# Performance work log

Hardware: AMD Instinct MI355X
Metric: run time of the kernel (lower is better)

## Reference

```python
import jax, jax.numpy as jnp
import numpy as np

Y, Z, H, R = 32, 64, 256, 256  # y_dim, z_dim, h_dim, rnn_dim
T, B = 200, 2048


def setup_inputs() -> dict:
    key = jax.random.key(0)
    ks = jax.random.split(key, 32)
    w = lambda k, shape: jax.random.normal(k, shape, jnp.float32) * 0.05
    z32 = lambda n: jnp.zeros((n,), jnp.float32)
    return {
        "states": jax.random.normal(ks[0], (T, B, Y), jnp.float32),
        "eps": jax.random.normal(ks[1], (T - 1, B, Z), jnp.float32),
        # encoder q(z|x,y,h): Linear(2Y+R,H) ReLU Linear(H,H) ReLU
        "enc_w1": w(ks[2], (H, 2 * Y + R)), "enc_b1": z32(H),
        "enc_w2": w(ks[3], (H, H)), "enc_b2": z32(H),
        "enc_mw": w(ks[4], (Z, H)), "enc_mb": z32(Z),
        "enc_sw": w(ks[5], (Z, H)), "enc_sb": z32(Z),
        # prior p(z|y,h): Linear(Y+R,H) ReLU Linear(H,H) ReLU
        "pri_w1": w(ks[6], (H, Y + R)), "pri_b1": z32(H),
        "pri_w2": w(ks[7], (H, H)), "pri_b2": z32(H),
        "pri_mw": w(ks[8], (Z, H)), "pri_mb": z32(Z),
        "pri_sw": w(ks[9], (Z, H)), "pri_sb": z32(Z),
        # decoder p(x|y,z,h): Linear(Y+Z+R,H) ReLU Linear(H,H) ReLU
        "dec_w1": w(ks[10], (H, Y + Z + R)), "dec_b1": z32(H),
        "dec_w2": w(ks[11], (H, H)), "dec_b2": z32(H),
        "dec_mw": w(ks[12], (Y, H)), "dec_mb": z32(Y),
        "dec_sw": w(ks[13], (Y, H)), "dec_sb": z32(Y),
        # GRU(Y+Z -> R), 1 layer; torch gate order [r, z, n]
        "gru_wih": w(ks[14], (3 * R, Y + Z)), "gru_whh": w(ks[15], (3 * R, R)),
        "gru_bih": z32(3 * R), "gru_bhh": z32(3 * R),
    }


def reference(states, eps, enc_w1, enc_b1, enc_w2, enc_b2, enc_mw, enc_mb,
              enc_sw, enc_sb, pri_w1, pri_b1, pri_w2, pri_b2, pri_mw, pri_mb,
              pri_sw, pri_sb, dec_w1, dec_b1, dec_w2, dec_b2, dec_mw, dec_mb,
              dec_sw, dec_sb, gru_wih, gru_whh, gru_bih, gru_bhh):
    batch = states.shape[1]
    rnn_dim = gru_whh.shape[1]
    relu, sp = jax.nn.relu, jax.nn.softplus
    LOG2PI = jnp.float32(np.log(2.0 * np.pi))

    def mlp2(x, w1, b1, w2, b2):
        return relu(relu(x @ w1.T + b1) @ w2.T + b2)

    def step(h, inp):
        y, x, e = inp  # y=states[t], x=states[t+1], e: reparam noise
        enc_h = mlp2(jnp.concatenate([x, y, h], 1), enc_w1, enc_b1, enc_w2, enc_b2)
        em = enc_h @ enc_mw.T + enc_mb
        es = sp(enc_h @ enc_sw.T + enc_sb)
        pri_h = mlp2(jnp.concatenate([y, h], 1), pri_w1, pri_b1, pri_w2, pri_b2)
        pm = pri_h @ pri_mw.T + pri_mb
        ps = sp(pri_h @ pri_sw.T + pri_sb)
        z = em + es * e  # sample_gauss
        dec_h = mlp2(jnp.concatenate([y, z, h], 1), dec_w1, dec_b1, dec_w2, dec_b2)
        dm = dec_h @ dec_mw.T + dec_mb
        ds = sp(dec_h @ dec_sw.T + dec_sb)
        # GRU cell (torch gate order r,z,n)
        gi = jnp.concatenate([x, z], 1) @ gru_wih.T + gru_bih
        gh = h @ gru_whh.T + gru_bhh
        ir, iz, inn = jnp.split(gi, 3, axis=1)
        hr, hz, hn = jnp.split(gh, 3, axis=1)
        r = jax.nn.sigmoid(ir + hr)
        u = jax.nn.sigmoid(iz + hz)
        n = jnp.tanh(inn + r * hn)
        h_new = (1.0 - u) * n + u * h
        kl = 0.5 * jnp.sum(2.0 * jnp.log(ps / es) + (es ** 2 + (em - pm) ** 2) / ps ** 2 - 1.0)
        nll = jnp.sum(jnp.log(ds) + (x - dm) ** 2 / (2.0 * ds ** 2) + 0.5 * LOG2PI)
        return h_new, (kl, nll)

    h0 = jnp.zeros((batch, rnn_dim), states.dtype)
    _, (kls, nlls) = jax.lax.scan(step, h0, (states[:-1], states[1:], eps))
    # out = [kl_loss, recon_loss]
    return jnp.stack([jnp.sum(kls), jnp.sum(nlls)])
```

## Files before the change

kernel.cpp:

```cpp
#include <hip/hip_runtime.h>

typedef unsigned short u16;
typedef unsigned int u32;
typedef __bf16 bf16x8 __attribute__((ext_vector_type(8)));
typedef float f32x4 __attribute__((ext_vector_type(4)));

#define YD 32
#define ZD 64
#define HD 256
#define RD 256
#define TSTEPS 199
#define BB 2048
#define MROWS 32
#define NBLK 64
#define NTHR 512
#define CATS 392
#define HBS  264

enum : int {
  OFF_ENC_W1 = 0,
  OFF_ENC_W2 = 81920,
  OFF_ENC_H  = 147456,
  OFF_PRI_W1 = 180224,
  OFF_PRI_W2 = 253952,
  OFF_PRI_H  = 319488,
  OFF_DEC_W1 = 352256,
  OFF_DEC_W2 = 442368,
  OFF_DEC_H  = 507904,
  OFF_GWIH   = 524288,
  OFF_GWHH   = 598016,
};

__device__ __forceinline__ u16 f2bf(float f) {
  u32 u = __float_as_uint(f);
  u += 0x7fffu + ((u >> 16) & 1u);
  return (u16)(u >> 16);
}
__device__ __forceinline__ float softplus_f(float x) {
  float l = __logf(1.f + __expf(-fabsf(x)));
  return x > 0.f ? x + l : l;
}
__device__ __forceinline__ float sigmoid_f(float x) {
  return __builtin_amdgcn_rcpf(1.f + __expf(-x));
}
__device__ __forceinline__ float tanh_f(float x) {
  float e = __expf(-2.f * fabsf(x));
  float t = (1.f - e) * __builtin_amdgcn_rcpf(1.f + e);
  return x >= 0.f ? t : -t;
}

template<int NT, int RT, int KS, int AS>
__device__ __forceinline__ void gemm_seg(f32x4 (&acc)[NT][RT],
    const u16* __restrict__ W, const int Kw, const int wrow0, const int wk0,
    const u16* A, const int acol0, const int rt0, const int lane)
{
  const int n = lane & 15, quad = lane >> 4;
  #pragma unroll
  for (int ks = 0; ks < KS; ++ks) {
    bf16x8 a[RT];
    #pragma unroll
    for (int rt = 0; rt < RT; ++rt)
      a[rt] = *reinterpret_cast<const bf16x8*>(A + ((rt0 + rt) * 16 + n) * AS + acol0 + ks * 32 + quad * 8);
    #pragma unroll
    for (int nt = 0; nt < NT; ++nt) {
      bf16x8 b = *reinterpret_cast<const bf16x8*>(W + (size_t)(wrow0 + nt * 16 + n) * Kw + wk0 + ks * 32 + quad * 8);
      #pragma unroll
      for (int rt = 0; rt < RT; ++rt)
        acc[nt][rt] = __builtin_amdgcn_mfma_f32_16x16x32_bf16(a[rt], b, acc[nt][rt], 0, 0, 0);
    }
  }
}

template<int NT, int RT, int DS>
__device__ __forceinline__ void store_relu(const f32x4 (&acc)[NT][RT], u16* dst,
    const int col0, const int rt0, const float* __restrict__ bias, const int lane)
{
  const int n = lane & 15, quad = lane >> 4;
  #pragma unroll
  for (int nt = 0; nt < NT; ++nt) {
    const float b = bias[col0 + nt * 16 + n];
    #pragma unroll
    for (int rt = 0; rt < RT; ++rt)
      #pragma unroll
      for (int i = 0; i < 4; ++i) {
        float v = fmaxf(acc[nt][rt][i] + b, 0.f);
        dst[((rt0 + rt) * 16 + quad * 4 + i) * DS + col0 + nt * 16 + n] = f2bf(v);
      }
  }
}

struct PrepArgs { const float* src[14]; int off[14]; int cnt[14]; };

__global__ void prep_weights(PrepArgs a, u16* __restrict__ dst) {
  const int j = blockIdx.y;
  const float* __restrict__ s = a.src[j];
  u16* d = dst + a.off[j];
  const int nel = a.cnt[j];
  for (int i = blockIdx.x * blockDim.x + threadIdx.x; i < nel; i += gridDim.x * blockDim.x)
    d[i] = f2bf(s[i]);
}

__global__ void zero_out_k(float* out) { if (threadIdx.x < 2) out[threadIdx.x] = 0.f; }

__global__ __launch_bounds__(NTHR, 1)
void vrnn_kernel(const float* __restrict__ states, const float* __restrict__ eps,
                 const float* __restrict__ enc_b1, const float* __restrict__ enc_b2,
                 const float* __restrict__ enc_mb, const float* __restrict__ enc_sb,
                 const float* __restrict__ pri_b1, const float* __restrict__ pri_b2,
                 const float* __restrict__ pri_mb, const float* __restrict__ pri_sb,
                 const float* __restrict__ dec_b1, const float* __restrict__ dec_b2,
                 const float* __restrict__ dec_mb, const float* __restrict__ dec_sb,
                 const float* __restrict__ gbih, const float* __restrict__ gbhh,
                 const u16* __restrict__ ws, float* __restrict__ out)
{
  __shared__ u16 cat[MROWS * CATS];
  __shared__ u16 hb1[MROWS * HBS];
  __shared__ u16 hb2[MROWS * HBS];

  const int tid = threadIdx.x;
  const int w = tid >> 6, lane = tid & 63;
  const int n = lane & 15, quad = lane >> 4;
  const int r0 = blockIdx.x * MROWS;
  const int n0 = w * 32;
  const int ctH = w & 3, rtH = w >> 2;

  for (int i = tid; i < MROWS * (HD / 2); i += NTHR) {
    int row = i >> 7, c = (i & 127) * 2;
    *reinterpret_cast<u32*>(&cat[row * CATS + 128 + c]) = 0u;
  }

  float hreg[2][2][4];
  #pragma unroll
  for (int a = 0; a < 2; ++a)
    #pragma unroll
    for (int b = 0; b < 2; ++b)
      #pragma unroll
      for (int c = 0; c < 4; ++c) hreg[a][b][c] = 0.f;

  float kl_acc = 0.f, nll_acc = 0.f;
  float emv[4], esv[4];

  for (int t = 0; t < TSTEPS; ++t) {
    {
      const int tt = tid & 255, row = tt >> 3, c4 = (tt & 7) * 4;
      const size_t tsel = (tid < 256) ? (size_t)(t + 1) : (size_t)t;
      const float4 v = *reinterpret_cast<const float4*>(states + (tsel * BB + r0 + row) * YD + c4);
      u16* d = cat + row * CATS + ((tid < 256) ? 0 : 32) + c4;
      d[0] = f2bf(v.x); d[1] = f2bf(v.y); d[2] = f2bf(v.z); d[3] = f2bf(v.w);
    }
    __syncthreads();

    {
      f32x4 acc[2][2] = {};
      gemm_seg<2, 2, 2, CATS>(acc, ws + OFF_ENC_W1, 320, n0, 0, cat, 0, 0, lane);
      gemm_seg<2, 2, 8, CATS>(acc, ws + OFF_ENC_W1, 320, n0, 64, cat, 128, 0, lane);
      store_relu<2, 2, HBS>(acc, hb1, n0, 0, enc_b1, lane);
    }
    __syncthreads();

    {
      f32x4 acc[2][2] = {};
      gemm_seg<2, 2, 8, HBS>(acc, ws + OFF_ENC_W2, 256, n0, 0, hb1, 0, 0, lane);
      store_relu<2, 2, HBS>(acc, hb2, n0, 0, enc_b2, lane);
    }
    __syncthreads();

    {
      f32x4 am[1][1] = {}, as[1][1] = {};
      gemm_seg<1, 1, 8, HBS>(am, ws + OFF_ENC_H, 256, ctH * 16, 0, hb2, 0, rtH, lane);
      gemm_seg<1, 1, 8, HBS>(as, ws + OFF_ENC_H, 256, 64 + ctH * 16, 0, hb2, 0, rtH, lane);
      const int j = ctH * 16 + n;
      #pragma unroll
      for (int i = 0; i < 4; ++i) {
        const int m = rtH * 16 + quad * 4 + i;
        float em = am[0][0][i] + enc_mb[j];
        float es = softplus_f(as[0][0][i] + enc_sb[j]);
        emv[i] = em; esv[i] = es;
        float e = eps[((size_t)t * BB + r0 + m) * ZD + j];
        cat[m * CATS + 64 + j] = f2bf(em + es * e);
      }
      f32x4 acc[2][2] = {};
      gemm_seg<2, 2, 1, CATS>(acc, ws + OFF_PRI_W1, 288, n0, 0, cat, 32, 0, lane);
      gemm_seg<2, 2, 8, CATS>(acc, ws + OFF_PRI_W1, 288, n0, 32, cat, 128, 0, lane);
      store_relu<2, 2, HBS>(acc, hb1, n0, 0, pri_b1, lane);
    }
    __syncthreads();

    {
      f32x4 acc[2][2] = {};
      gemm_seg<2, 2, 8, HBS>(acc, ws + OFF_PRI_W2, 256, n0, 0, hb1, 0, 0, lane);
      store_relu<2, 2, HBS>(acc, hb2, n0, 0, pri_b2, lane);
    }
    __syncthreads();

    {
      f32x4 am[1][1] = {}, as[1][1] = {};
      gemm_seg<1, 1, 8, HBS>(am, ws + OFF_PRI_H, 256, ctH * 16, 0, hb2, 0, rtH, lane);
      gemm_seg<1, 1, 8, HBS>(as, ws + OFF_PRI_H, 256, 64 + ctH * 16, 0, hb2, 0, rtH, lane);
      const int j = ctH * 16 + n;
      #pragma unroll
      for (int i = 0; i < 4; ++i) {
        float pm = am[0][0][i] + pri_mb[j];
        float ps = softplus_f(as[0][0][i] + pri_sb[j]);
        float es = esv[i], em = emv[i];
        float d = em - pm;
        kl_acc += 0.5f * (2.f * __logf(ps * __builtin_amdgcn_rcpf(es))
                          + (es * es + d * d) / (ps * ps) - 1.f);
      }
      f32x4 acc[2][2] = {};
      gemm_seg<2, 2, 3, CATS>(acc, ws + OFF_DEC_W1, 352, n0, 0, cat, 32, 0, lane);
      gemm_seg<2, 2, 8, CATS>(acc, ws + OFF_DEC_W1, 352, n0, 96, cat, 128, 0, lane);
      store_relu<2, 2, HBS>(acc, hb1, n0, 0, dec_b1, lane);
    }
    __syncthreads();

    {
      f32x4 acc[2][2] = {};
      gemm_seg<2, 2, 8, HBS>(acc, ws + OFF_DEC_W2, 256, n0, 0, hb1, 0, 0, lane);
      store_relu<2, 2, HBS>(acc, hb2, n0, 0, dec_b2, lane);
    }
    __syncthreads();

    {
      if (w < 4) {
        const int p = w & 1, rtb = w >> 1;
        f32x4 am[1][1] = {}, as[1][1] = {};
        gemm_seg<1, 1, 8, HBS>(am, ws + OFF_DEC_H, 256, p * 16, 0, hb2, 0, rtb, lane);
        gemm_seg<1, 1, 8, HBS>(as, ws + OFF_DEC_H, 256, 32 + p * 16, 0, hb2, 0, rtb, lane);
        const int j = p * 16 + n;
        #pragma unroll
        for (int i = 0; i < 4; ++i) {
          const int m = rtb * 16 + quad * 4 + i;
          float dm = am[0][0][i] + dec_mb[j];
          float ds = softplus_f(as[0][0][i] + dec_sb[j]);
          float xv = states[((size_t)(t + 1) * BB + r0 + m) * YD + j];
          float dd = xv - dm;
          nll_acc += __logf(ds) + dd * dd / (2.f * ds * ds) + 0.91893853320467274178f;
        }
      }
      f32x4 aR[2][2] = {}, aU[2][2] = {}, aN[2][2] = {}, aH[2][2] = {};
      gemm_seg<2, 2, 1, CATS>(aR, ws + OFF_GWIH, 96, n0, 0, cat, 0, 0, lane);
      gemm_seg<2, 2, 2, CATS>(aR, ws + OFF_GWIH, 96, n0, 32, cat, 64, 0, lane);
      gemm_seg<2, 2, 8, CATS>(aR, ws + OFF_GWHH, 256, n0, 0, cat, 128, 0, lane);
      gemm_seg<2, 2, 1, CATS>(aU, ws + OFF_GWIH, 96, RD + n0, 0, cat, 0, 0, lane);
      gemm_seg<2, 2, 2, CATS>(aU, ws + OFF_GWIH, 96, RD + n0, 32, cat, 64, 0, lane);
      gemm_seg<2, 2, 8, CATS>(aU, ws + OFF_GWHH, 256, RD + n0, 0, cat, 128, 0, lane);
      gemm_seg<2, 2, 1, CATS>(aN, ws + OFF_GWIH, 96, 2 * RD + n0, 0, cat, 0, 0, lane);
      gemm_seg<2, 2, 2, CATS>(aN, ws + OFF_GWIH, 96, 2 * RD + n0, 32, cat, 64, 0, lane);
      gemm_seg<2, 2, 8, CATS>(aH, ws + OFF_GWHH, 256, 2 * RD + n0, 0, cat, 128, 0, lane);
      #pragma unroll
      for (int nt = 0; nt < 2; ++nt) {
        const int j = n0 + nt * 16 + n;
        const float br = gbih[j] + gbhh[j];
        const float bu = gbih[RD + j] + gbhh[RD + j];
        const float bin = gbih[2 * RD + j];
        const float bhn = gbhh[2 * RD + j];
        #pragma unroll
        for (int rt = 0; rt < 2; ++rt)
          #pragma unroll
          for (int i = 0; i < 4; ++i) {
            float r = sigmoid_f(aR[nt][rt][i] + br);
            float u = sigmoid_f(aU[nt][rt][i] + bu);
            float nn = tanh_f(aN[nt][rt][i] + bin + r * (aH[nt][rt][i] + bhn));
            hreg[nt][rt][i] = (1.f - u) * nn + u * hreg[nt][rt][i];
          }
      }
    }
    __syncthreads();

    #pragma unroll
    for (int nt = 0; nt < 2; ++nt)
      #pragma unroll
      for (int rt = 0; rt < 2; ++rt)
        #pragma unroll
        for (int i = 0; i < 4; ++i)
          cat[(rt * 16 + quad * 4 + i) * CATS + 128 + n0 + nt * 16 + n] = f2bf(hreg[nt][rt][i]);
  }

  float kv = kl_acc, nv = nll_acc;
  #pragma unroll
  for (int off = 32; off > 0; off >>= 1) {
    kv += __shfl_down(kv, off, 64);
    nv += __shfl_down(nv, off, 64);
  }
  if (lane == 0) {
    atomicAdd(out + 0, kv);
    atomicAdd(out + 1, nv);
  }
}

extern "C" void kernel_launch(void* const* d_in, const int* in_sizes, int n_in,
                              void* d_out, int out_size, void* d_ws, size_t ws_size,
                              hipStream_t stream) {
  const float* states = (const float*)d_in[0];
  const float* eps    = (const float*)d_in[1];
  u16* ws   = (u16*)d_ws;
  float* out = (float*)d_out;

  PrepArgs pa;
  const int jsrc[14] = {2, 4, 6, 8, 10, 12, 14, 16, 18, 20, 22, 24, 26, 27};
  const int joff[14] = {OFF_ENC_W1, OFF_ENC_W2, OFF_ENC_H, OFF_ENC_H + 16384,
                        OFF_PRI_W1, OFF_PRI_W2, OFF_PRI_H, OFF_PRI_H + 16384,
                        OFF_DEC_W1, OFF_DEC_W2, OFF_DEC_H, OFF_DEC_H + 8192,
                        OFF_GWIH, OFF_GWHH};
  const int jcnt[14] = {81920, 65536, 16384, 16384,
                        73728, 65536, 16384, 16384,
                        90112, 65536, 8192, 8192,
                        73728, 196608};
  for (int j = 0; j < 14; ++j) {
    pa.src[j] = (const float*)d_in[jsrc[j]];
    pa.off[j] = joff[j];
    pa.cnt[j] = jcnt[j];
  }

  zero_out_k<<<dim3(1), dim3(64), 0, stream>>>(out);
  prep_weights<<<dim3(64, 14), dim3(256), 0, stream>>>(pa, ws);
  vrnn_kernel<<<dim3(NBLK), dim3(NTHR), 0, stream>>>(
      states, eps,
      (const float*)d_in[3],  (const float*)d_in[5],
      (const float*)d_in[7],  (const float*)d_in[9],
      (const float*)d_in[11], (const float*)d_in[13],
      (const float*)d_in[15], (const float*)d_in[17],
      (const float*)d_in[19], (const float*)d_in[21],
      (const float*)d_in[23], (const float*)d_in[25],
      (const float*)d_in[28], (const float*)d_in[29],
      ws, out);
}
```

Measured before the change: 11.13 ms.

## Double rows per block to reuse weights and prefetch per-step inputs

Each block now handles 64 batch rows instead of 32, so every weight fragment loaded from global memory feeds four row tiles of MFMAs instead of two. This halves the grid to 32 blocks. Biases are hoisted into registers, the next step's states and the current eps/x values are prefetched ahead of the GEMMs, and the GRU gate computation is reordered to reduce live accumulator registers. The cost is fewer blocks on a large GPU, larger LDS buffers and more register pressure, all on a latency-bound recurrent loop.

```diff
diff --git a/kernel.cpp b/kernel.cpp
--- a/kernel.cpp
+++ b/kernel.cpp
@@ -11,8 +11,8 @@
 #define RD 256
 #define TSTEPS 199
 #define BB 2048
-#define MROWS 32
-#define NBLK 64
+#define MROWS 64
+#define NBLK 32
 #define NTHR 512
 #define CATS 392
 #define HBS  264
@@ -73,12 +73,12 @@
 
 template<int NT, int RT, int DS>
 __device__ __forceinline__ void store_relu(const f32x4 (&acc)[NT][RT], u16* dst,
-    const int col0, const int rt0, const float* __restrict__ bias, const int lane)
+    const int col0, const int rt0, const float* bias_r, const int lane)
 {
   const int n = lane & 15, quad = lane >> 4;
   #pragma unroll
   for (int nt = 0; nt < NT; ++nt) {
-    const float b = bias[col0 + nt * 16 + n];
+    const float b = bias_r[nt];
     #pragma unroll
     for (int rt = 0; rt < RT; ++rt)
       #pragma unroll
@@ -102,7 +102,7 @@
 
 __global__ void zero_out_k(float* out) { if (threadIdx.x < 2) out[threadIdx.x] = 0.f; }
 
-__global__ __launch_bounds__(NTHR, 1)
+__global__ __launch_bounds__(NTHR, 2)
 void vrnn_kernel(const float* __restrict__ states, const float* __restrict__ eps,
                  const float* __restrict__ enc_b1, const float* __restrict__ enc_b2,
                  const float* __restrict__ enc_mb, const float* __restrict__ enc_sb,
@@ -122,156 +122,203 @@
   const int n = lane & 15, quad = lane >> 4;
   const int r0 = blockIdx.x * MROWS;
   const int n0 = w * 32;
-  const int ctH = w & 3, rtH = w >> 2;
+  const int ctH = w & 3, rtH0 = (w >> 2) * 2;
+  const int pD = w & 1, rtD = w >> 1;
+
+  float b1e[2], b2e[2], b1p[2], b2p[2], b1d[2], b2d[2];
+  float brg[2], bug[2], bing[2], bhng[2];
+  #pragma unroll
+  for (int nt = 0; nt < 2; ++nt) {
+    const int j = n0 + nt * 16 + n;
+    b1e[nt] = enc_b1[j]; b2e[nt] = enc_b2[j];
+    b1p[nt] = pri_b1[j]; b2p[nt] = pri_b2[j];
+    b1d[nt] = dec_b1[j]; b2d[nt] = dec_b2[j];
+    brg[nt] = gbih[j] + gbhh[j];
+    bug[nt] = gbih[RD + j] + gbhh[RD + j];
+    bing[nt] = gbih[2 * RD + j];
+    bhng[nt] = gbhh[2 * RD + j];
+  }
+  const int jH = ctH * 16 + n;
+  const float bem = enc_mb[jH], bes = enc_sb[jH];
+  const float bpm = pri_mb[jH], bps = pri_sb[jH];
+  const int jD = pD * 16 + n;
+  const float bdm = dec_mb[jD], bds = dec_sb[jD];
 
   for (int i = tid; i < MROWS * (HD / 2); i += NTHR) {
     int row = i >> 7, c = (i & 127) * 2;
     *reinterpret_cast<u32*>(&cat[row * CATS + 128 + c]) = 0u;
   }
 
-  float hreg[2][2][4];
+  float hreg[2][4][4];
   #pragma unroll
   for (int a = 0; a < 2; ++a)
     #pragma unroll
-    for (int b = 0; b < 2; ++b)
+    for (int b = 0; b < 4; ++b)
       #pragma unroll
       for (int c = 0; c < 4; ++c) hreg[a][b][c] = 0.f;
 
+  const int srow = tid >> 3, sc4 = (tid & 7) * 4;
+  float4 xf = *reinterpret_cast<const float4*>(states + ((size_t)1 * BB + r0 + srow) * YD + sc4);
+  float4 yf = *reinterpret_cast<const float4*>(states + ((size_t)0 * BB + r0 + srow) * YD + sc4);
+
   float kl_acc = 0.f, nll_acc = 0.f;
-  float emv[4], esv[4];
 
   for (int t = 0; t < TSTEPS; ++t) {
     {
-      const int tt = tid & 255, row = tt >> 3, c4 = (tt & 7) * 4;
-      const size_t tsel = (tid < 256) ? (size_t)(t + 1) : (size_t)t;
-      const float4 v = *reinterpret_cast<const float4*>(states + (tsel * BB + r0 + row) * YD + c4);
-      u16* d = cat + row * CATS + ((tid < 256) ? 0 : 32) + c4;
-      d[0] = f2bf(v.x); d[1] = f2bf(v.y); d[2] = f2bf(v.z); d[3] = f2bf(v.w);
-    }
-    __syncthreads();
-
-    {
-      f32x4 acc[2][2] = {};
-      gemm_seg<2, 2, 2, CATS>(acc, ws + OFF_ENC_W1, 320, n0, 0, cat, 0, 0, lane);
-      gemm_seg<2, 2, 8, CATS>(acc, ws + OFF_ENC_W1, 320, n0, 64, cat, 128, 0, lane);
-      store_relu<2, 2, HBS>(acc, hb1, n0, 0, enc_b1, lane);
-    }
-    __syncthreads();
-
-    {
-      f32x4 acc[2][2] = {};
-      gemm_seg<2, 2, 8, HBS>(acc, ws + OFF_ENC_W2, 256, n0, 0, hb1, 0, 0, lane);
-      store_relu<2, 2, HBS>(acc, hb2, n0, 0, enc_b2, lane);
+      u16* dx = cat + srow * CATS + sc4;
+      dx[0] = f2bf(xf.x); dx[1] = f2bf(xf.y); dx[2] = f2bf(xf.z); dx[3] = f2bf(xf.w);
+      u16* dy = cat + srow * CATS + 32 + sc4;
+      dy[0] = f2bf(yf.x); dy[1] = f2bf(yf.y); dy[2] = f2bf(yf.z); dy[3] = f2bf(yf.w);
+    }
+    __syncthreads();
+
+    float ev[2][4];
+    #pragma unroll
+    for (int rt = 0; rt < 2; ++rt)
+      #pragma unroll
+      for (int i = 0; i < 4; ++i)
+        ev[rt][i] = eps[((size_t)t * BB + r0 + (rtH0 + rt) * 16 + quad * 4 + i) * ZD + jH];
+    float xs[4];
+    #pragma unroll
+    for (int i = 0; i < 4; ++i)
+      xs[i] = states[((size_t)(t + 1) * BB + r0 + rtD * 16 + quad * 4 + i) * YD + jD];
+
+    {
+      f32x4 acc[2][4] = {};
+      gemm_seg<2, 4, 2, CATS>(acc, ws + OFF_ENC_W1, 320, n0, 0, cat, 0, 0, lane);
+      gemm_seg<2, 4, 8, CATS>(acc, ws + OFF_ENC_W1, 320, n0, 64, cat, 128, 0, lane);
+      store_relu<2, 4, HBS>(acc, hb1, n0, 0, b1e, lane);
+    }
+    __syncthreads();
+
+    {
+      f32x4 acc[2][4] = {};
+      gemm_seg<2, 4, 8, HBS>(acc, ws + OFF_ENC_W2, 256, n0, 0, hb1, 0, 0, lane);
+      store_relu<2, 4, HBS>(acc, hb2, n0, 0, b2e, lane);
+    }
+    __syncthreads();
+
+    float emv[2][4], esv[2][4];
+    {
+      f32x4 am[1][2] = {}, as[1][2] = {};
+      gemm_seg<1, 2, 8, HBS>(am, ws + OFF_ENC_H, 256, ctH * 16, 0, hb2, 0, rtH0, lane);
+      gemm_seg<1, 2, 8, HBS>(as, ws + OFF_ENC_H, 256, 64 + ctH * 16, 0, hb2, 0, rtH0, lane);
+      #pragma unroll
+      for (int rt = 0; rt < 2; ++rt)
+        #pragma unroll
+        for (int i = 0; i < 4; ++i) {
+          const int m = (rtH0 + rt) * 16 + quad * 4 + i;
+          float em = am[0][rt][i] + bem;
+          float es = softplus_f(as[0][rt][i] + bes);
+          emv[rt][i] = em; esv[rt][i] = es;
+          cat[m * CATS + 64 + jH] = f2bf(em + es * ev[rt][i]);
+        }
+      f32x4 acc[2][4] = {};
+      gemm_seg<2, 4, 1, CATS>(acc, ws + OFF_PRI_W1, 288, n0, 0, cat, 32, 0, lane);
+      gemm_seg<2, 4, 8, CATS>(acc, ws + OFF_PRI_W1, 288, n0, 32, cat, 128, 0, lane);
+      store_relu<2, 4, HBS>(acc, hb1, n0, 0, b1p, lane);
+    }
+    __syncthreads();
+
+    {
+      f32x4 acc[2][4] = {};
+      gemm_seg<2, 4, 8, HBS>(acc, ws + OFF_PRI_W2, 256, n0, 0, hb1, 0, 0, lane);
+      store_relu<2, 4, HBS>(acc, hb2, n0, 0, b2p, lane);
+    }
+    __syncthreads();
+
+    {
+      f32x4 am[1][2] = {}, as[1][2] = {};
+      gemm_seg<1, 2, 8, HBS>(am, ws + OFF_PRI_H, 256, ctH * 16, 0, hb2, 0, rtH0, lane);
+      gemm_seg<1, 2, 8, HBS>(as, ws + OFF_PRI_H, 256, 64 + ctH * 16, 0, hb2, 0, rtH0, lane);
+      #pragma unroll
+      for (int rt = 0; rt < 2; ++rt)
+        #pragma unroll
+        for (int i = 0; i < 4; ++i) {
+          float pm = am[0][rt][i] + bpm;
+          float ps = softplus_f(as[0][rt][i] + bps);
+          float es = esv[rt][i], em = emv[rt][i];
+          float d = em - pm;
+          kl_acc += 0.5f * (2.f * __logf(ps * __builtin_amdgcn_rcpf(es))
+                            + (es * es + d * d) / (ps * ps) - 1.f);
+        }
+      f32x4 acc[2][4] = {};
+      gemm_seg<2, 4, 3, CATS>(acc, ws + OFF_DEC_W1, 352, n0, 0, cat, 32, 0, lane);
+      gemm_seg<2, 4, 8, CATS>(acc, ws + OFF_DEC_W1, 352, n0, 96, cat, 128, 0, lane);
+      store_relu<2, 4, HBS>(acc, hb1, n0, 0, b1d, lane);
+    }
+    __syncthreads();
+
+    {
+      f32x4 acc[2][4] = {};
+      gemm_seg<2, 4, 8, HBS>(acc, ws + OFF_DEC_W2, 256, n0, 0, hb1, 0, 0, lane);
+      store_relu<2, 4, HBS>(acc, hb2, n0, 0, b2d, lane);
     }
     __syncthreads();
 
     {
       f32x4 am[1][1] = {}, as[1][1] = {};
-      gemm_seg<1, 1, 8, HBS>(am, ws + OFF_ENC_H, 256, ctH * 16, 0, hb2, 0, rtH, lane);
-      gemm_seg<1, 1, 8, HBS>(as, ws + OFF_ENC_H, 256, 64 + ctH * 16, 0, hb2, 0, rtH, lane);
-      const int j = ctH * 16 + n;
+      gemm_seg<1, 1, 8, HBS>(am, ws + OFF_DEC_H, 256, pD * 16, 0, hb2, 0, rtD, lane);
+      gemm_seg<1, 1, 8, HBS>(as, ws + OFF_DEC_H, 256, 32 + pD * 16, 0, hb2, 0, rtD, lane);
       #pragma unroll
       for (int i = 0; i < 4; ++i) {
-        const int m = rtH * 16 + quad * 4 + i;
-        float em = am[0][0][i] + enc_mb[j];
-        float es = softplus_f(as[0][0][i] + enc_sb[j]);
-        emv[i] = em; esv[i] = es;
-        float e = eps[((size_t)t * BB + r0 + m) * ZD + j];
-        cat[m * CATS + 64 + j] = f2bf(em + es * e);
-      }
-      f32x4 acc[2][2] = {};
-      gemm_seg<2, 2, 1, CATS>(acc, ws + OFF_PRI_W1, 288, n0, 0, cat, 32, 0, lane);
-      gemm_seg<2, 2, 8, CATS>(acc, ws + OFF_PRI_W1, 288, n0, 32, cat, 128, 0, lane);
-      store_relu<2, 2, HBS>(acc, hb1, n0, 0, pri_b1, lane);
-    }
-    __syncthreads();
-
-    {
-      f32x4 acc[2][2] = {};
-      gemm_seg<2, 2, 8, HBS>(acc, ws + OFF_PRI_W2, 256, n0, 0, hb1, 0, 0, lane);
-      store_relu<2, 2, HBS>(acc, hb2, n0, 0, pri_b2, lane);
-    }
-    __syncthreads();
-
-    {
-      f32x4 am[1][1] = {}, as[1][1] = {};
-      gemm_seg<1, 1, 8, HBS>(am, ws + OFF_PRI_H, 256, ctH * 16, 0, hb2, 0, rtH, lane);
-      gemm_seg<1, 1, 8, HBS>(as, ws + OFF_PRI_H, 256, 64 + ctH * 16, 0, hb2, 0, rtH, lane);
-      const int j = ctH * 16 + n;
-      #pragma unroll
-      for (int i = 0; i < 4; ++i) {
-        float pm = am[0][0][i] + pri_mb[j];
-        float ps = softplus_f(as[0][0][i] + pri_sb[j]);
-        float es = esv[i], em = emv[i];
-        float d = em - pm;
-        kl_acc += 0.5f * (2.f * __logf(ps * __builtin_amdgcn_rcpf(es))
-                          + (es * es + d * d) / (ps * ps) - 1.f);
-      }
-      f32x4 acc[2][2] = {};
-      gemm_seg<2, 2, 3, CATS>(acc, ws + OFF_DEC_W1, 352, n0, 0, cat, 32, 0, lane);
-      gemm_seg<2, 2, 8, CATS>(acc, ws + OFF_DEC_W1, 352, n0, 96, cat, 128, 0, lane);
-      store_relu<2, 2, HBS>(acc, hb1, n0, 0, dec_b1, lane);
-    }
-    __syncthreads();
-
-    {
-      f32x4 acc[2][2] = {};
-      gemm_seg<2, 2, 8, HBS>(acc, ws + OFF_DEC_W2, 256, n0, 0, hb1, 0, 0, lane);
-      store_relu<2, 2, HBS>(acc, hb2, n0, 0, dec_b2, lane);
-    }
-    __syncthreads();
-
-    {
-      if (w < 4) {
-        const int p = w & 1, rtb = w >> 1;
-        f32x4 am[1][1] = {}, as[1][1] = {};
-        gemm_seg<1, 1, 8, HBS>(am, ws + OFF_DEC_H, 256, p * 16, 0, hb2, 0, rtb, lane);
-        gemm_seg<1, 1, 8, HBS>(as, ws + OFF_DEC_H, 256, 32 + p * 16, 0, hb2, 0, rtb, lane);
-        const int j = p * 16 + n;
-        #pragma unroll
-        for (int i = 0; i < 4; ++i) {
-          const int m = rtb * 16 + quad * 4 + i;
-          float dm = am[0][0][i] + dec_mb[j];
-          float ds = softplus_f(as[0][0][i] + dec_sb[j]);
-          float xv = states[((size_t)(t + 1) * BB + r0 + m) * YD + j];
-          float dd = xv - dm;
-          nll_acc += __logf(ds) + dd * dd / (2.f * ds * ds) + 0.91893853320467274178f;
-        }
-      }
-      f32x4 aR[2][2] = {}, aU[2][2] = {}, aN[2][2] = {}, aH[2][2] = {};
-      gemm_seg<2, 2, 1, CATS>(aR, ws + OFF_GWIH, 96, n0, 0, cat, 0, 0, lane);
-      gemm_seg<2, 2, 2, CATS>(aR, ws + OFF_GWIH, 96, n0, 32, cat, 64, 0, lane);
-      gemm_seg<2, 2, 8, CATS>(aR, ws + OFF_GWHH, 256, n0, 0, cat, 128, 0, lane);
-      gemm_seg<2, 2, 1, CATS>(aU, ws + OFF_GWIH, 96, RD + n0, 0, cat, 0, 0, lane);
-      gemm_seg<2, 2, 2, CATS>(aU, ws + OFF_GWIH, 96, RD + n0, 32, cat, 64, 0, lane);
-      gemm_seg<2, 2, 8, CATS>(aU, ws + OFF_GWHH, 256, RD + n0, 0, cat, 128, 0, lane);
-      gemm_seg<2, 2, 1, CATS>(aN, ws + OFF_GWIH, 96, 2 * RD + n0, 0, cat, 0, 0, lane);
-      gemm_seg<2, 2, 2, CATS>(aN, ws + OFF_GWIH, 96, 2 * RD + n0, 32, cat, 64, 0, lane);
-      gemm_seg<2, 2, 8, CATS>(aH, ws + OFF_GWHH, 256, 2 * RD + n0, 0, cat, 128, 0, lane);
-      #pragma unroll
-      for (int nt = 0; nt < 2; ++nt) {
-        const int j = n0 + nt * 16 + n;
-        const float br = gbih[j] + gbhh[j];
-        const float bu = gbih[RD + j] + gbhh[RD + j];
-        const float bin = gbih[2 * RD + j];
-        const float bhn = gbhh[2 * RD + j];
-        #pragma unroll
-        for (int rt = 0; rt < 2; ++rt)
+        float dm = am[0][0][i] + bdm;
+        float ds = softplus_f(as[0][0][i] + bds);
+        float dd = xs[i] - dm;
+        nll_acc += __logf(ds) + dd * dd / (2.f * ds * ds) + 0.91893853320467274178f;
+      }
+      f32x4 aH[2][4] = {};
+      gemm_seg<2, 4, 8, CATS>(aH, ws + OFF_GWHH, 256, 2 * RD + n0, 0, cat, 128, 0, lane);
+      {
+        f32x4 aR[2][4] = {};
+        gemm_seg<2, 4, 1, CATS>(aR, ws + OFF_GWIH, 96, n0, 0, cat, 0, 0, lane);
+        gemm_seg<2, 4, 2, CATS>(aR, ws + OFF_GWIH, 96, n0, 32, cat, 64, 0, lane);
+        gemm_seg<2, 4, 8, CATS>(aR, ws + OFF_GWHH, 256, n0, 0, cat, 128, 0, lane);
+        #pragma unroll
+        for (int nt = 0; nt < 2; ++nt)
           #pragma unroll
-          for (int i = 0; i < 4; ++i) {
-            float r = sigmoid_f(aR[nt][rt][i] + br);
-            float u = sigmoid_f(aU[nt][rt][i] + bu);
-            float nn = tanh_f(aN[nt][rt][i] + bin + r * (aH[nt][rt][i] + bhn));
-            hreg[nt][rt][i] = (1.f - u) * nn + u * hreg[nt][rt][i];
-          }
-      }
+          for (int rt = 0; rt < 4; ++rt)
+            #pragma unroll
+            for (int i = 0; i < 4; ++i)
+              aH[nt][rt][i] = sigmoid_f(aR[nt][rt][i] + brg[nt]) * (aH[nt][rt][i] + bhng[nt]);
+      }
+      {
+        f32x4 aN[2][4] = {};
+        gemm_seg<2, 4, 1, CATS>(aN, ws + OFF_GWIH, 96, 2 * RD + n0, 0, cat, 0, 0, lane);
+        gemm_seg<2, 4, 2, CATS>(aN, ws + OFF_GWIH, 96, 2 * RD + n0, 32, cat, 64, 0, lane);
+        #pragma unroll
+        for (int nt = 0; nt < 2; ++nt)
+          #pragma unroll
+          for (int rt = 0; rt < 4; ++rt)
+            #pragma unroll
+            for (int i = 0; i < 4; ++i)
+              aH[nt][rt][i] = tanh_f(aN[nt][rt][i] + bing[nt] + aH[nt][rt][i]);
+      }
+      {
+        f32x4 aU[2][4] = {};
+        gemm_seg<2, 4, 1, CATS>(aU, ws + OFF_GWIH, 96, RD + n0, 0, cat, 0, 0, lane);
+        gemm_seg<2, 4, 2, CATS>(aU, ws + OFF_GWIH, 96, RD + n0, 32, cat, 64, 0, lane);
+        gemm_seg<2, 4, 8, CATS>(aU, ws + OFF_GWHH, 256, RD + n0, 0, cat, 128, 0, lane);
+        #pragma unroll
+        for (int nt = 0; nt < 2; ++nt)
+          #pragma unroll
+          for (int rt = 0; rt < 4; ++rt)
+            #pragma unroll
+            for (int i = 0; i < 4; ++i) {
+              float u = sigmoid_f(aU[nt][rt][i] + bug[nt]);
+              hreg[nt][rt][i] = (1.f - u) * aH[nt][rt][i] + u * hreg[nt][rt][i];
+            }
+      }
+      const int tn = (t + 1 < TSTEPS) ? t + 1 : TSTEPS - 1;
+      xf = *reinterpret_cast<const float4*>(states + ((size_t)(tn + 1) * BB + r0 + srow) * YD + sc4);
+      yf = *reinterpret_cast<const float4*>(states + ((size_t)tn * BB + r0 + srow) * YD + sc4);
     }
     __syncthreads();
 
     #pragma unroll
     for (int nt = 0; nt < 2; ++nt)
       #pragma unroll
-      for (int rt = 0; rt < 2; ++rt)
+      for (int rt = 0; rt < 4; ++rt)
         #pragma unroll
         for (int i = 0; i < 4; ++i)
           cat[(rt * 16 + quad * 4 + i) * CATS + 128 + n0 + nt * 16 + n] = f2bf(hreg[nt][rt][i]);
```

Result: slower. 14.90 ms (+33.9%).

## Double threads per block, split head GEMMs across waves, prefetch states

Applied to the files above, without the earlier changes.

The block grows to 1024 threads and each wave handles 16 output columns instead of 32. The mean/std head GEMMs are split across all waves, with results staged in new shared buffers and read back for the KL, NLL and z computations. States for the next step and eps are prefetched into registers ahead of use, biases are hoisted out of the time loop, and weight fragments are loaded up front inside gemm_seg. This adds a few barriers and rounds the head outputs to bf16 in exchange for more parallelism per step. It also raises register pressure from the preloaded weights.

```diff
diff --git a/kernel.cpp b/kernel.cpp
--- a/kernel.cpp
+++ b/kernel.cpp
@@ -13,9 +13,11 @@
 #define BB 2048
 #define MROWS 32
 #define NBLK 64
-#define NTHR 512
+#define NTHR 1024
 #define CATS 392
 #define HBS  264
+#define HES  136
+#define HDS  72
 
 enum : int {
   OFF_ENC_W1 = 0,
@@ -36,6 +38,9 @@
   u += 0x7fffu + ((u >> 16) & 1u);
   return (u16)(u >> 16);
 }
+__device__ __forceinline__ float bf2f(u16 b) {
+  return __uint_as_float((u32)b << 16);
+}
 __device__ __forceinline__ float softplus_f(float x) {
   float l = __logf(1.f + __expf(-fabsf(x)));
   return x > 0.f ? x + l : l;
@@ -55,6 +60,14 @@
     const u16* A, const int acol0, const int rt0, const int lane)
 {
   const int n = lane & 15, quad = lane >> 4;
+  bf16x8 b[KS][NT];
+  #pragma unroll
+  for (int nt = 0; nt < NT; ++nt) {
+    const u16* wp = W + (size_t)(wrow0 + nt * 16 + n) * Kw + wk0 + quad * 8;
+    #pragma unroll
+    for (int ks = 0; ks < KS; ++ks)
+      b[ks][nt] = *reinterpret_cast<const bf16x8*>(wp + ks * 32);
+  }
   #pragma unroll
   for (int ks = 0; ks < KS; ++ks) {
     bf16x8 a[RT];
@@ -62,31 +75,25 @@
     for (int rt = 0; rt < RT; ++rt)
       a[rt] = *reinterpret_cast<const bf16x8*>(A + ((rt0 + rt) * 16 + n) * AS + acol0 + ks * 32 + quad * 8);
     #pragma unroll
-    for (int nt = 0; nt < NT; ++nt) {
-      bf16x8 b = *reinterpret_cast<const bf16x8*>(W + (size_t)(wrow0 + nt * 16 + n) * Kw + wk0 + ks * 32 + quad * 8);
+    for (int nt = 0; nt < NT; ++nt)
       #pragma unroll
       for (int rt = 0; rt < RT; ++rt)
-        acc[nt][rt] = __builtin_amdgcn_mfma_f32_16x16x32_bf16(a[rt], b, acc[nt][rt], 0, 0, 0);
-    }
-  }
-}
-
-template<int NT, int RT, int DS>
-__device__ __forceinline__ void store_relu(const f32x4 (&acc)[NT][RT], u16* dst,
-    const int col0, const int rt0, const float* __restrict__ bias, const int lane)
+        acc[nt][rt] = __builtin_amdgcn_mfma_f32_16x16x32_bf16(a[rt], b[ks][nt], acc[nt][rt], 0, 0, 0);
+  }
+}
+
+template<int RT, int DS>
+__device__ __forceinline__ void store_relu(const f32x4 (&acc)[1][RT], u16* dst,
+    const int col0, const int rt0, const float bias, const int lane)
 {
   const int n = lane & 15, quad = lane >> 4;
   #pragma unroll
-  for (int nt = 0; nt < NT; ++nt) {
-    const float b = bias[col0 + nt * 16 + n];
-    #pragma unroll
-    for (int rt = 0; rt < RT; ++rt)
-      #pragma unroll
-      for (int i = 0; i < 4; ++i) {
-        float v = fmaxf(acc[nt][rt][i] + b, 0.f);
-        dst[((rt0 + rt) * 16 + quad * 4 + i) * DS + col0 + nt * 16 + n] = f2bf(v);
-      }
-  }
+  for (int rt = 0; rt < RT; ++rt)
+    #pragma unroll
+    for (int i = 0; i < 4; ++i) {
+      float v = fmaxf(acc[0][rt][i] + bias, 0.f);
+      dst[((rt0 + rt) * 16 + quad * 4 + i) * DS + col0 + n] = f2bf(v);
+    }
 }
 
 struct PrepArgs { const float* src[14]; int off[14]; int cnt[14]; };
@@ -102,7 +109,7 @@
 
 __global__ void zero_out_k(float* out) { if (threadIdx.x < 2) out[threadIdx.x] = 0.f; }
 
-__global__ __launch_bounds__(NTHR, 1)
+__global__ __launch_bounds__(NTHR, 4)
 void vrnn_kernel(const float* __restrict__ states, const float* __restrict__ eps,
                  const float* __restrict__ enc_b1, const float* __restrict__ enc_b2,
                  const float* __restrict__ enc_mb, const float* __restrict__ enc_sb,
@@ -116,165 +123,215 @@
   __shared__ u16 cat[MROWS * CATS];
   __shared__ u16 hb1[MROWS * HBS];
   __shared__ u16 hb2[MROWS * HBS];
+  __shared__ u16 hbhE[MROWS * HES];
+  __shared__ u16 hbhP[MROWS * HES];
+  __shared__ u16 hbhD[MROWS * HDS];
 
   const int tid = threadIdx.x;
   const int w = tid >> 6, lane = tid & 63;
   const int n = lane & 15, quad = lane >> 4;
   const int r0 = blockIdx.x * MROWS;
-  const int n0 = w * 32;
-  const int ctH = w & 3, rtH = w >> 2;
+  const int n0 = w * 16;
+  const int cgE = w & 7, rtE = w >> 3;
+  const int cgD = w & 3, rtD = (w >> 2) & 1;
+
+  const int jW = n0 + n;
+  const float b1e = enc_b1[jW], b2e = enc_b2[jW];
+  const float b1p = pri_b1[jW], b2p = pri_b2[jW];
+  const float b1d = dec_b1[jW], b2d = dec_b2[jW];
+  const float brg = gbih[jW] + gbhh[jW];
+  const float bug = gbih[RD + jW] + gbhh[RD + jW];
+  const float bing = gbih[2 * RD + jW];
+  const float bhng = gbhh[2 * RD + jW];
+  const float bhE = (cgE < 4) ? enc_mb[cgE * 16 + n] : enc_sb[(cgE - 4) * 16 + n];
+  const float bhP = (cgE < 4) ? pri_mb[cgE * 16 + n] : pri_sb[(cgE - 4) * 16 + n];
+  const float bhD = (cgD < 2) ? dec_mb[cgD * 16 + n] : dec_sb[(cgD - 2) * 16 + n];
 
   for (int i = tid; i < MROWS * (HD / 2); i += NTHR) {
     int row = i >> 7, c = (i & 127) * 2;
     *reinterpret_cast<u32*>(&cat[row * CATS + 128 + c]) = 0u;
   }
 
-  float hreg[2][2][4];
+  float hreg[2][4];
   #pragma unroll
   for (int a = 0; a < 2; ++a)
     #pragma unroll
-    for (int b = 0; b < 2; ++b)
-      #pragma unroll
-      for (int c = 0; c < 4; ++c) hreg[a][b][c] = 0.f;
+    for (int c = 0; c < 4; ++c) hreg[a][c] = 0.f;
+
+  const int srow = (tid & 255) >> 3, sc4 = (tid & 7) * 4;
+  float4 xyf = make_float4(0.f, 0.f, 0.f, 0.f);
+  if (tid < 512)
+    xyf = *reinterpret_cast<const float4*>(states + ((size_t)((tid < 256) ? 1 : 0) * BB + r0 + srow) * YD + sc4);
+
+  const int mz = tid >> 5, jz = (tid & 31) * 2;
+  const int mn = (tid & 511) >> 4, jn = (tid & 15) * 2;
 
   float kl_acc = 0.f, nll_acc = 0.f;
-  float emv[4], esv[4];
 
   for (int t = 0; t < TSTEPS; ++t) {
-    {
-      const int tt = tid & 255, row = tt >> 3, c4 = (tt & 7) * 4;
-      const size_t tsel = (tid < 256) ? (size_t)(t + 1) : (size_t)t;
-      const float4 v = *reinterpret_cast<const float4*>(states + (tsel * BB + r0 + row) * YD + c4);
-      u16* d = cat + row * CATS + ((tid < 256) ? 0 : 32) + c4;
-      d[0] = f2bf(v.x); d[1] = f2bf(v.y); d[2] = f2bf(v.z); d[3] = f2bf(v.w);
-    }
-    __syncthreads();
-
-    {
-      f32x4 acc[2][2] = {};
-      gemm_seg<2, 2, 2, CATS>(acc, ws + OFF_ENC_W1, 320, n0, 0, cat, 0, 0, lane);
-      gemm_seg<2, 2, 8, CATS>(acc, ws + OFF_ENC_W1, 320, n0, 64, cat, 128, 0, lane);
-      store_relu<2, 2, HBS>(acc, hb1, n0, 0, enc_b1, lane);
-    }
-    __syncthreads();
-
-    {
-      f32x4 acc[2][2] = {};
-      gemm_seg<2, 2, 8, HBS>(acc, ws + OFF_ENC_W2, 256, n0, 0, hb1, 0, 0, lane);
-      store_relu<2, 2, HBS>(acc, hb2, n0, 0, enc_b2, lane);
-    }
-    __syncthreads();
-
-    {
-      f32x4 am[1][1] = {}, as[1][1] = {};
-      gemm_seg<1, 1, 8, HBS>(am, ws + OFF_ENC_H, 256, ctH * 16, 0, hb2, 0, rtH, lane);
-      gemm_seg<1, 1, 8, HBS>(as, ws + OFF_ENC_H, 256, 64 + ctH * 16, 0, hb2, 0, rtH, lane);
-      const int j = ctH * 16 + n;
+    if (tid < 512) {
+      u16* d = cat + srow * CATS + ((tid < 256) ? 0 : 32) + sc4;
+      d[0] = f2bf(xyf.x); d[1] = f2bf(xyf.y); d[2] = f2bf(xyf.z); d[3] = f2bf(xyf.w);
+    }
+    float2 ev2 = *reinterpret_cast<const float2*>(eps + ((size_t)t * BB + r0 + mz) * ZD + jz);
+    float2 xs2 = make_float2(0.f, 0.f);
+    if (tid < 512)
+      xs2 = *reinterpret_cast<const float2*>(states + ((size_t)(t + 1) * BB + r0 + mn) * YD + jn);
+    __syncthreads();
+
+    {
+      f32x4 acc[1][2] = {};
+      gemm_seg<1, 2, 2, CATS>(acc, ws + OFF_ENC_W1, 320, n0, 0, cat, 0, 0, lane);
+      gemm_seg<1, 2, 8, CATS>(acc, ws + OFF_ENC_W1, 320, n0, 64, cat, 128, 0, lane);
+      store_relu<2, HBS>(acc, hb1, n0, 0, b1e, lane);
+    }
+    __syncthreads();
+
+    {
+      f32x4 acc[1][2] = {};
+      gemm_seg<1, 2, 8, HBS>(acc, ws + OFF_ENC_W2, 256, n0, 0, hb1, 0, 0, lane);
+      store_relu<2, HBS>(acc, hb2, n0, 0, b2e, lane);
+    }
+    __syncthreads();
+
+    {
+      f32x4 acc[1][1] = {};
+      gemm_seg<1, 1, 8, HBS>(acc, ws + OFF_ENC_H, 256, cgE * 16, 0, hb2, 0, rtE, lane);
       #pragma unroll
       for (int i = 0; i < 4; ++i) {
-        const int m = rtH * 16 + quad * 4 + i;
-        float em = am[0][0][i] + enc_mb[j];
-        float es = softplus_f(as[0][0][i] + enc_sb[j]);
-        emv[i] = em; esv[i] = es;
-        float e = eps[((size_t)t * BB + r0 + m) * ZD + j];
-        cat[m * CATS + 64 + j] = f2bf(em + es * e);
-      }
-      f32x4 acc[2][2] = {};
-      gemm_seg<2, 2, 1, CATS>(acc, ws + OFF_PRI_W1, 288, n0, 0, cat, 32, 0, lane);
-      gemm_seg<2, 2, 8, CATS>(acc, ws + OFF_PRI_W1, 288, n0, 32, cat, 128, 0, lane);
-      store_relu<2, 2, HBS>(acc, hb1, n0, 0, pri_b1, lane);
-    }
-    __syncthreads();
-
-    {
-      f32x4 acc[2][2] = {};
-      gemm_seg<2, 2, 8, HBS>(acc, ws + OFF_PRI_W2, 256, n0, 0, hb1, 0, 0, lane);
-      store_relu<2, 2, HBS>(acc, hb2, n0, 0, pri_b2, lane);
-    }
-    __syncthreads();
-
-    {
-      f32x4 am[1][1] = {}, as[1][1] = {};
-      gemm_seg<1, 1, 8, HBS>(am, ws + OFF_PRI_H, 256, ctH * 16, 0, hb2, 0, rtH, lane);
-      gemm_seg<1, 1, 8, HBS>(as, ws + OFF_PRI_H, 256, 64 + ctH * 16, 0, hb2, 0, rtH, lane);
-      const int j = ctH * 16 + n;
+        float v = acc[0][0][i] + bhE;
+        if (cgE >= 4) v = softplus_f(v);
+        hbhE[(rtE * 16 + quad * 4 + i) * HES + cgE * 16 + n] = f2bf(v);
+      }
+    }
+    __syncthreads();
+
+    {
+      float em0 = bf2f(hbhE[mz * HES + jz]);
+      float em1 = bf2f(hbhE[mz * HES + jz + 1]);
+      float es0 = bf2f(hbhE[mz * HES + 64 + jz]);
+      float es1 = bf2f(hbhE[mz * HES + 64 + jz + 1]);
+      cat[mz * CATS + 64 + jz] = f2bf(em0 + es0 * ev2.x);
+      cat[mz * CATS + 64 + jz + 1] = f2bf(em1 + es1 * ev2.y);
+      f32x4 acc[1][2] = {};
+      gemm_seg<1, 2, 1, CATS>(acc, ws + OFF_PRI_W1, 288, n0, 0, cat, 32, 0, lane);
+      gemm_seg<1, 2, 8, CATS>(acc, ws + OFF_PRI_W1, 288, n0, 32, cat, 128, 0, lane);
+      store_relu<2, HBS>(acc, hb1, n0, 0, b1p, lane);
+    }
+    __syncthreads();
+
+    {
+      f32x4 acc[1][2] = {};
+      gemm_seg<1, 2, 8, HBS>(acc, ws + OFF_PRI_W2, 256, n0, 0, hb1, 0, 0, lane);
+      store_relu<2, HBS>(acc, hb2, n0, 0, b2p, lane);
+    }
+    __syncthreads();
+
+    {
+      f32x4 acc[1][1] = {};
+      gemm_seg<1, 1, 8, HBS>(acc, ws + OFF_PRI_H, 256, cgE * 16, 0, hb2, 0, rtE, lane);
       #pragma unroll
       for (int i = 0; i < 4; ++i) {
-        float pm = am[0][0][i] + pri_mb[j];
-        float ps = softplus_f(as[0][0][i] + pri_sb[j]);
-        float es = esv[i], em = emv[i];
+        float v = acc[0][0][i] + bhP;
+        if (cgE >= 4) v = softplus_f(v);
+        hbhP[(rtE * 16 + quad * 4 + i) * HES + cgE * 16 + n] = f2bf(v);
+      }
+    }
+    __syncthreads();
+
+    {
+      #pragma unroll
+      for (int c = 0; c < 2; ++c) {
+        float em = bf2f(hbhE[mz * HES + jz + c]);
+        float es = bf2f(hbhE[mz * HES + 64 + jz + c]);
+        float pm = bf2f(hbhP[mz * HES + jz + c]);
+        float ps = bf2f(hbhP[mz * HES + 64 + jz + c]);
         float d = em - pm;
         kl_acc += 0.5f * (2.f * __logf(ps * __builtin_amdgcn_rcpf(es))
                           + (es * es + d * d) / (ps * ps) - 1.f);
       }
-      f32x4 acc[2][2] = {};
-      gemm_seg<2, 2, 3, CATS>(acc, ws + OFF_DEC_W1, 352, n0, 0, cat, 32, 0, lane);
-      gemm_seg<2, 2, 8, CATS>(acc, ws + OFF_DEC_W1, 352, n0, 96, cat, 128, 0, lane);
-      store_relu<2, 2, HBS>(acc, hb1, n0, 0, dec_b1, lane);
-    }
-    __syncthreads();
-
-    {
-      f32x4 acc[2][2] = {};
-      gemm_seg<2, 2, 8, HBS>(acc, ws + OFF_DEC_W2, 256, n0, 0, hb1, 0, 0, lane);
-      store_relu<2, 2, HBS>(acc, hb2, n0, 0, dec_b2, lane);
-    }
-    __syncthreads();
-
-    {
-      if (w < 4) {
-        const int p = w & 1, rtb = w >> 1;
-        f32x4 am[1][1] = {}, as[1][1] = {};
-        gemm_seg<1, 1, 8, HBS>(am, ws + OFF_DEC_H, 256, p * 16, 0, hb2, 0, rtb, lane);
-        gemm_seg<1, 1, 8, HBS>(as, ws + OFF_DEC_H, 256, 32 + p * 16, 0, hb2, 0, rtb, lane);
-        const int j = p * 16 + n;
+      f32x4 acc[1][2] = {};
+      gemm_seg<1, 2, 3, CATS>(acc, ws + OFF_DEC_W1, 352, n0, 0, cat, 32, 0, lane);
+      gemm_seg<1, 2, 8, CATS>(acc, ws + OFF_DEC_W1, 352, n0, 96, cat, 128, 0, lane);
+      store_relu<2, HBS>(acc, hb1, n0, 0, b1d, lane);
+    }
+    __syncthreads();
+
+    {
+      f32x4 acc[1][2] = {};
+      gemm_seg<1, 2, 8, HBS>(acc, ws + OFF_DEC_W2, 256, n0, 0, hb1, 0, 0, lane);
+      store_relu<2, HBS>(acc, hb2, n0, 0, b2d, lane);
+    }
+    __syncthreads();
+
+    {
+      if (w < 8) {
+        f32x4 acc[1][1] = {};
+        gemm_seg<1, 1, 8, HBS>(acc, ws + OFF_DEC_H, 256, cgD * 16, 0, hb2, 0, rtD, lane);
         #pragma unroll
         for (int i = 0; i < 4; ++i) {
-          const int m = rtb * 16 + quad * 4 + i;
-          float dm = am[0][0][i] + dec_mb[j];
-          float ds = softplus_f(as[0][0][i] + dec_sb[j]);
-          float xv = states[((size_t)(t + 1) * BB + r0 + m) * YD + j];
-          float dd = xv - dm;
-          nll_acc += __logf(ds) + dd * dd / (2.f * ds * ds) + 0.91893853320467274178f;
+          float v = acc[0][0][i] + bhD;
+          if (cgD >= 2) v = softplus_f(v);
+          hbhD[(rtD * 16 + quad * 4 + i) * HDS + cgD * 16 + n] = f2bf(v);
         }
       }
-      f32x4 aR[2][2] = {}, aU[2][2] = {}, aN[2][2] = {}, aH[2][2] = {};
-      gemm_seg<2, 2, 1, CATS>(aR, ws + OFF_GWIH, 96, n0, 0, cat, 0, 0, lane);
-      gemm_seg<2, 2, 2, CATS>(aR, ws + OFF_GWIH, 96, n0, 32, cat, 64, 0, lane);
-      gemm_seg<2, 2, 8, CATS>(aR, ws + OFF_GWHH, 256, n0, 0, cat, 128, 0, lane);
-      gemm_seg<2, 2, 1, CATS>(aU, ws + OFF_GWIH, 96, RD + n0, 0, cat, 0, 0, lane);
-      gemm_seg<2, 2, 2, CATS>(aU, ws + OFF_GWIH, 96, RD + n0, 32, cat, 64, 0, lane);
-      gemm_seg<2, 2, 8, CATS>(aU, ws + OFF_GWHH, 256, RD + n0, 0, cat, 128, 0, lane);
-      gemm_seg<2, 2, 1, CATS>(aN, ws + OFF_GWIH, 96, 2 * RD + n0, 0, cat, 0, 0, lane);
-      gemm_seg<2, 2, 2, CATS>(aN, ws + OFF_GWIH, 96, 2 * RD + n0, 32, cat, 64, 0, lane);
-      gemm_seg<2, 2, 8, CATS>(aH, ws + OFF_GWHH, 256, 2 * RD + n0, 0, cat, 128, 0, lane);
-      #pragma unroll
-      for (int nt = 0; nt < 2; ++nt) {
-        const int j = n0 + nt * 16 + n;
-        const float br = gbih[j] + gbhh[j];
-        const float bu = gbih[RD + j] + gbhh[RD + j];
-        const float bin = gbih[2 * RD + j];
-        const float bhn = gbhh[2 * RD + j];
+      f32x4 aH[1][2] = {};
+      gemm_seg<1, 2, 8, CATS>(aH, ws + OFF_GWHH, 256, 2 * RD + n0, 0, cat, 128, 0, lane);
+      {
+        f32x4 aR[1][2] = {};
+        gemm_seg<1, 2, 1, CATS>(aR, ws + OFF_GWIH, 96, n0, 0, cat, 0, 0, lane);
+        gemm_seg<1, 2, 2, CATS>(aR, ws + OFF_GWIH, 96, n0, 32, cat, 64, 0, lane);
+        gemm_seg<1, 2, 8, CATS>(aR, ws + OFF_GWHH, 256, n0, 0, cat, 128, 0, lane);
+        #pragma unroll
+        for (int rt = 0; rt < 2; ++rt)
+          #pragma unroll
+          for (int i = 0; i < 4; ++i)
+            aH[0][rt][i] = sigmoid_f(aR[0][rt][i] + brg) * (aH[0][rt][i] + bhng);
+      }
+      {
+        f32x4 aN[1][2] = {};
+        gemm_seg<1, 2, 1, CATS>(aN, ws + OFF_GWIH, 96, 2 * RD + n0, 0, cat, 0, 0, lane);
+        gemm_seg<1, 2, 2, CATS>(aN, ws + OFF_GWIH, 96, 2 * RD + n0, 32, cat, 64, 0, lane);
+        #pragma unroll
+        for (int rt = 0; rt < 2; ++rt)
+          #pragma unroll
+          for (int i = 0; i < 4; ++i)
+            aH[0][rt][i] = tanh_f(aN[0][rt][i] + bing + aH[0][rt][i]);
+      }
+      {
+        f32x4 aU[1][2] = {};
+        gemm_seg<1, 2, 1, CATS>(aU, ws + OFF_GWIH, 96, RD + n0, 0, cat, 0, 0, lane);
+        gemm_seg<1, 2, 2, CATS>(aU, ws + OFF_GWIH, 96, RD + n0, 32, cat, 64, 0, lane);
+        gemm_seg<1, 2, 8, CATS>(aU, ws + OFF_GWHH, 256, RD + n0, 0, cat, 128, 0, lane);
         #pragma unroll
         for (int rt = 0; rt < 2; ++rt)
           #pragma unroll
           for (int i = 0; i < 4; ++i) {
-            float r = sigmoid_f(aR[nt][rt][i] + br);
-            float u = sigmoid_f(aU[nt][rt][i] + bu);
-            float nn = tanh_f(aN[nt][rt][i] + bin + r * (aH[nt][rt][i] + bhn));
-            hreg[nt][rt][i] = (1.f - u) * nn + u * hreg[nt][rt][i];
+            float u = sigmoid_f(aU[0][rt][i] + bug);
+            hreg[rt][i] = (1.f - u) * aH[0][rt][i] + u * hreg[rt][i];
           }
       }
-    }
-    __syncthreads();
-
-    #pragma unroll
-    for (int nt = 0; nt < 2; ++nt)
-      #pragma unroll
-      for (int rt = 0; rt < 2; ++rt)
-        #pragma unroll
-        for (int i = 0; i < 4; ++i)
-          cat[(rt * 16 + quad * 4 + i) * CATS + 128 + n0 + nt * 16 + n] = f2bf(hreg[nt][rt][i]);
+      const int tn = (t + 1 < TSTEPS) ? t + 1 : TSTEPS - 1;
+      if (tid < 512)
+        xyf = *reinterpret_cast<const float4*>(states + ((size_t)((tid < 256) ? tn + 1 : tn) * BB + r0 + srow) * YD + sc4);
+    }
+    __syncthreads();
+
+    if (tid < 512) {
+      #pragma unroll
+      for (int c = 0; c < 2; ++c) {
+        float dm = bf2f(hbhD[mn * HDS + jn + c]);
+        float ds = bf2f(hbhD[mn * HDS + 32 + jn + c]);
+        float xv = (c == 0) ? xs2.x : xs2.y;
+        float dd = xv - dm;
+        nll_acc += __logf(ds) + dd * dd / (2.f * ds * ds) + 0.91893853320467274178f;
+      }
+    }
+    #pragma unroll
+    for (int rt = 0; rt < 2; ++rt)
+      #pragma unroll
+      for (int i = 0; i < 4; ++i)
+        cat[(rt * 16 + quad * 4 + i) * CATS + 128 + n0 + n] = f2bf(hreg[rt][i]);
   }
 
   float kv = kl_acc, nv = nll_acc;
```

Measured after the change: 10.77 ms. 1.03x faster.
